# Performance work log

Measured on AMD Instinct MI355X. Metric: run time of the kernel, lower is better.

The kernel has to match this reference:

```python
import jax, jax.numpy as jnp
import numpy as np
from math import log, sqrt

B, S, D, H, L = 16, 512, 512, 8, 6
DPH = D // H
DFF = 2048
VOCAB = 1024
MAXDEG = 64
NPC, NS = 4096, 4096


def setup_inputs() -> dict:
    rng = np.random.default_rng(0)
    raw_x = rng.integers(0, VOCAB + 1, (B, S)).astype(np.int32)
    scatter_degree = rng.integers(0, MAXDEG + 1, (B, S)).astype(np.int32)

    def uniq_triples(n, seed):
        r = np.random.default_rng(seed)
        flat = r.choice(B * S * S, n, replace=False)  # unique (b,i,j)
        b, i, j = np.unravel_index(flat, (B, S, S))
        return np.stack([b, i, j], 1).astype(np.int32)

    parentchild_indices = uniq_triples(NPC, 1)
    silbing_indices = uniq_triples(NS, 2)
    parent_child_now = np.stack([np.arange(B), rng.integers(0, S, B)], 1).astype(np.int32)
    silbing_now = np.stack([np.arange(B), rng.integers(0, S, B)], 1).astype(np.int32)

    key = jax.random.key(0)
    ks = jax.random.split(key, 16)
    sc = 0.02
    inp = {
        "raw_x": jnp.asarray(raw_x),
        "scatter_degree": jnp.asarray(scatter_degree),
        "parentchild_indices": jnp.asarray(parentchild_indices),
        "parent_child_now": jnp.asarray(parent_child_now),
        "silbing_indices": jnp.asarray(silbing_indices),
        "silbing_now": jnp.asarray(silbing_now),
        "vocab_emb": jax.random.normal(ks[0], (VOCAB + 1, D), jnp.float32) * sc,
        "degree_emb": jax.random.normal(ks[1], (MAXDEG + 1, D), jnp.float32) * sc,
        "active_rel_emb": jax.random.normal(ks[2], (2, D), jnp.float32) * sc,
        "relation_encoder": jax.random.uniform(ks[3], (3,), jnp.float32),
        "Wq": jax.random.normal(ks[4], (L, D, D), jnp.float32) * sc,
        "bq": jnp.zeros((L, D), jnp.float32),
        "Wk": jax.random.normal(ks[5], (L, D, D), jnp.float32) * sc,
        "bk": jnp.zeros((L, D), jnp.float32),
        "Wv": jax.random.normal(ks[6], (L, D, D), jnp.float32) * sc,
        "bv": jnp.zeros((L, D), jnp.float32),
        "Wo": jax.random.normal(ks[7], (L, D, D), jnp.float32) * sc,
        "bo": jnp.zeros((L, D), jnp.float32),
        "W1": jax.random.normal(ks[8], (L, DFF, D), jnp.float32) * sc,
        "b1": jnp.zeros((L, DFF), jnp.float32),
        "W2": jax.random.normal(ks[9], (L, D, DFF), jnp.float32) * sc,
        "b2": jnp.zeros((L, D), jnp.float32),
        "ln_g": jnp.ones((L, D), jnp.float32),
        "ln_b": jnp.zeros((L, D), jnp.float32),
        "logits_w": jax.random.normal(ks[10], (VOCAB, D), jnp.float32) * sc,
    }
    return inp


def _layer_norm(x, g, b):
    m = jnp.mean(x, -1, keepdims=True)
    v = jnp.mean((x - m) ** 2, -1, keepdims=True)  # biased var, eps=1e-5 (torch default)
    return (x - m) * jax.lax.rsqrt(v + 1e-5) * g + b


def _forward(raw_x, scatter_degree, parentchild_indices, parent_child_now,
             silbing_indices, silbing_now, vocab_emb, degree_emb, active_rel_emb,
             relation_encoder, Wq, bq, Wk, bk, Wv, bv, Wo, bo, W1, b1, W2, b2,
             ln_g, ln_b, logits_w):
    x = vocab_emb[raw_x]  # [B,S,D]
    # sinusoidal positional encoding
    pos = jnp.arange(S, dtype=jnp.float32)[:, None]
    div = jnp.exp(jnp.arange(0, D, 2, dtype=jnp.float32) * (-log(10000.0) / D))
    pe = jnp.zeros((S, D), x.dtype).at[:, 0::2].set(jnp.sin(pos * div)).at[:, 1::2].set(jnp.cos(pos * div))
    x = x + pe
    # structural encodings
    x = x + degree_emb[scatter_degree]
    x = x.at[parent_child_now[:, 0], parent_child_now[:, 1]].add(active_rel_emb[0])
    x = x.at[silbing_now[:, 0], silbing_now[:, 1]].add(active_rel_emb[1])

    pb, pi, pj = parentchild_indices[:, 0], parentchild_indices[:, 1], parentchild_indices[:, 2]
    sb, si, sj = silbing_indices[:, 0], silbing_indices[:, 1], silbing_indices[:, 2]
    inv_norm = 1.0 / sqrt(DPH)

    for l in range(L):
        q = (x @ Wq[l].T + bq[l]).reshape(B, S, H, DPH).transpose(0, 2, 1, 3)
        k = (x @ Wk[l].T + bk[l]).reshape(B, S, H, DPH).transpose(0, 2, 1, 3)
        v = (x @ Wv[l].T + bv[l]).reshape(B, S, H, DPH).transpose(0, 2, 1, 3)
        scores = jnp.einsum('bhqd,bhkd->bhqk', q, k) * inv_norm  # [B,H,S,S]
        # scatter-added relational bias (broadcast over all heads)
        scores = scores.at[pb, :, pi, pj].add(relation_encoder[0])
        scores = scores.at[pb, :, pj, pi].add(relation_encoder[1])
        scores = scores.at[sb, :, si, sj].add(relation_encoder[2])
        scores = scores.at[sb, :, sj, si].add(relation_encoder[2])
        attn = jax.nn.softmax(scores, axis=-1)
        o = jnp.einsum('bhqk,bhkd->bhqd', attn, v).transpose(0, 2, 1, 3).reshape(B, S, D)
        o = o @ Wo[l].T + bo[l]
        x = _layer_norm(x + o, ln_g[l], ln_b[l])
        ff = jax.nn.relu(x @ W1[l].T + b1[l]) @ W2[l].T + b2[l]
        x = _layer_norm(x + ff, ln_g[l], ln_b[l])

    return x[:, -1] @ logits_w.T  # [B, VOCAB]


def reference(raw_x, scatter_degree, parentchild_indices, parent_child_now,
              silbing_indices, silbing_now, vocab_emb, degree_emb, active_rel_emb,
              relation_encoder, Wq, bq, Wk, bk, Wv, bv, Wo, bo, W1, b1, W2, b2,
              ln_g, ln_b, logits_w):
    return _forward(raw_x, scatter_degree, parentchild_indices, parent_child_now,
                    silbing_indices, silbing_now, vocab_emb, degree_emb, active_rel_emb,
                    relation_encoder, Wq, bq, Wk, bk, Wv, bv, Wo, bo, W1, b1, W2, b2,
                    ln_g, ln_b, logits_w)
```

## Files before the change

### kernel.cpp

```cpp
#include <hip/hip_runtime.h>
#include <hip/hip_bf16.h>
#include <math.h>

#define B_ 16
#define S_ 512
#define D_ 512
#define H_ 8
#define L_ 6
#define DPH_ 64
#define DFF_ 2048
#define VOCAB_ 1024
#define NPC_ 4096
#define NS_ 4096
#define BS_ (B_ * S_)
#define LOG2E 1.4426950408889634f

typedef __attribute__((ext_vector_type(8))) short bf16x8;
typedef __attribute__((ext_vector_type(4))) float f32x4;

__device__ __forceinline__ ushort f2bf(float f) {
    __hip_bfloat16 h = __float2bfloat16(f);
    return __builtin_bit_cast(ushort, h);
}
__device__ __forceinline__ float bf2f(ushort u) {
    unsigned int v = ((unsigned int)u) << 16;
    return __builtin_bit_cast(float, v);
}

__global__ __launch_bounds__(256) void embed_kernel(
    const int* __restrict__ raw_x, const int* __restrict__ sdeg,
    const float* __restrict__ vemb, const float* __restrict__ demb,
    ushort* __restrict__ xb)
{
    size_t idx = (size_t)blockIdx.x * 256 + threadIdx.x;
    int d = (int)(idx & (D_ - 1));
    size_t bs = idx >> 9;
    int s = (int)(bs & (S_ - 1));
    int tok = raw_x[bs];
    int dg  = sdeg[bs];
    float e = expf(-(float)(d & ~1) * (9.210340371976184f / (float)D_));
    float ang = (float)s * e;
    float pe = (d & 1) ? cosf(ang) : sinf(ang);
    xb[idx] = f2bf(vemb[(size_t)tok * D_ + d] + pe + demb[(size_t)dg * D_ + d]);
}

__global__ void relnow_kernel(const int* __restrict__ pcn, const int* __restrict__ sbn,
                              const float* __restrict__ arel, ushort* __restrict__ xb)
{
    int b = blockIdx.x;
    int t = threadIdx.x;
    int b1 = pcn[b * 2 + 0], p1 = pcn[b * 2 + 1];
    size_t i1 = ((size_t)(b1 * S_ + p1)) * D_ + t;
    xb[i1] = f2bf(bf2f(xb[i1]) + arel[t]);
    int b2 = sbn[b * 2 + 0], p2 = sbn[b * 2 + 1];
    size_t i2 = ((size_t)(b2 * S_ + p2)) * D_ + t;
    xb[i2] = f2bf(bf2f(xb[i2]) + arel[D_ + t]);
}

__global__ void bias_scatter_kernel(const int* __restrict__ pc, const int* __restrict__ sb,
                                    const float* __restrict__ renc, float* __restrict__ bias)
{
    int t = blockIdx.x * 256 + threadIdx.x;
    float r0 = renc[0], r1 = renc[1], r2 = renc[2];
    if (t < NPC_) {
        int b = pc[t * 3 + 0], i = pc[t * 3 + 1], j = pc[t * 3 + 2];
        atomicAdd(&bias[((size_t)b * S_ + i) * S_ + j], r0);
        atomicAdd(&bias[((size_t)b * S_ + j) * S_ + i], r1);
    } else if (t < NPC_ + NS_) {
        int u = t - NPC_;
        int b = sb[u * 3 + 0], i = sb[u * 3 + 1], j = sb[u * 3 + 2];
        atomicAdd(&bias[((size_t)b * S_ + i) * S_ + j], r2);
        atomicAdd(&bias[((size_t)b * S_ + j) * S_ + i], r2);
    }
}

__global__ __launch_bounds__(256) void bias_cast_kernel(const float* __restrict__ src,
                                                        ushort* __restrict__ dst)
{
    int i = blockIdx.x * 256 + threadIdx.x;
    float4 v = ((const float4*)src)[i];
    ushort4 o;
    o.x = f2bf(v.x * LOG2E); o.y = f2bf(v.y * LOG2E);
    o.z = f2bf(v.z * LOG2E); o.w = f2bf(v.w * LOG2E);
    ((ushort4*)dst)[i] = o;
}

__global__ __launch_bounds__(256) void cast4_kernel(const float* __restrict__ src,
                                                    ushort* __restrict__ dst, int n4)
{
    int i = blockIdx.x * 256 + threadIdx.x;
    if (i >= n4) return;
    float4 v = ((const float4*)src)[i];
    ushort4 o;
    o.x = f2bf(v.x); o.y = f2bf(v.y); o.z = f2bf(v.z); o.w = f2bf(v.w);
    ((ushort4*)dst)[i] = o;
}

__global__ __launch_bounds__(256) void pack_qkv_kernel(
    const float* __restrict__ Wq, const float* __restrict__ Wk, const float* __restrict__ Wv,
    ushort* __restrict__ dst)
{
    int idx = blockIdx.x * 256 + threadIdx.x;
    int c = idx & 511;
    int rl = idx >> 9;
    int r = rl % 1536, l = rl / 1536;
    float v;
    if (r < 512)       v = Wq[((size_t)l * 512 + r) * 512 + c];
    else if (r < 1024) v = Wk[((size_t)l * 512 + (r - 512)) * 512 + c];
    else               v = Wv[((size_t)l * 512 + (r - 1024)) * 512 + c];
    dst[idx] = f2bf(v);
}

__global__ void pack_bqkv_kernel(const float* __restrict__ bq, const float* __restrict__ bk,
                                 const float* __restrict__ bv, float* __restrict__ dst)
{
    int idx = blockIdx.x * 256 + threadIdx.x;
    if (idx >= L_ * 1536) return;
    int r = idx % 1536, l = idx / 1536;
    float v;
    if (r < 512)       v = bq[l * 512 + r];
    else if (r < 1024) v = bk[l * 512 + r - 512];
    else               v = bv[l * 512 + r - 1024];
    dst[idx] = v;
}

#define GL2LDS(g, l) __builtin_amdgcn_global_load_lds( \
    (const __attribute__((address_space(1))) void*)(g), \
    (__attribute__((address_space(3))) void*)(l), 16, 0, 0)

#define STAGE_AB(AsX, BsX, kk) do {                                            \
    _Pragma("unroll")                                                          \
    for (int i_ = 0; i_ < 2; i_++) {                                           \
        int r_ = i_ * 64 + wv * 16;                                            \
        GL2LDS(A + (size_t)(row0 + r_ + lr) * K + (kk) + lk, &AsX[r_ * 32]);   \
        GL2LDS(W + (size_t)(col0 + r_ + lr) * K + (kk) + lk, &BsX[r_ * 32]);   \
    } } while (0)

#define COMPUTE_AB(AsX, BsX) do {                                              \
    bf16x8 af[4], bf[4];                                                       \
    _Pragma("unroll")                                                          \
    for (int mi = 0; mi < 4; mi++)                                             \
        af[mi] = *(const bf16x8*)&AsX[(wm * 64 + mi * 16 + lc) * 32 + lq * 8]; \
    _Pragma("unroll")                                                          \
    for (int ni = 0; ni < 4; ni++)                                             \
        bf[ni] = *(const bf16x8*)&BsX[(wn * 64 + ni * 16 + lc) * 32 + lq * 8]; \
    _Pragma("unroll")                                                          \
    for (int mi = 0; mi < 4; mi++)                                             \
        _Pragma("unroll")                                                      \
        for (int ni = 0; ni < 4; ni++)                                         \
            acc[mi][ni] = __builtin_amdgcn_mfma_f32_16x16x32_bf16(af[mi], bf[ni], acc[mi][ni], 0, 0, 0); \
    } while (0)

__global__ __launch_bounds__(256) void gemm_bf16(
    const ushort* __restrict__ A, const ushort* __restrict__ W,
    const float* __restrict__ bias, ushort* __restrict__ Cb,
    int K, int M, int mode)
{
    __shared__ ushort As0[128 * 32];
    __shared__ ushort As1[128 * 32];
    __shared__ ushort Bs0[128 * 32];
    __shared__ ushort Bs1[128 * 32];

    const int t  = threadIdx.x;
    const int wv = t >> 6;
    const int ln = t & 63;
    const int wm = wv >> 1, wn = wv & 1;
    const int lq = ln >> 4, lc = ln & 15;
    const int row0 = blockIdx.x * 128;
    const int col0 = blockIdx.y * 128;
    const int lr = ln >> 2;
    const int lk = (ln & 3) * 8;

    f32x4 acc[4][4] = {};
    const int nk = K >> 5;

    STAGE_AB(As0, Bs0, 0);
    for (int ki = 0; ki < nk; ki += 2) {
        __syncthreads();
        if (ki + 1 < nk) STAGE_AB(As1, Bs1, (ki + 1) << 5);
        COMPUTE_AB(As0, Bs0);
        __syncthreads();
        if (ki + 2 < nk) STAGE_AB(As0, Bs0, (ki + 2) << 5);
        COMPUTE_AB(As1, Bs1);
    }

    #pragma unroll
    for (int mi = 0; mi < 4; mi++) {
        #pragma unroll
        for (int ni = 0; ni < 4; ni++) {
            int gcol = col0 + wn * 64 + ni * 16 + lc;
            float bb = bias[gcol];
            #pragma unroll
            for (int rr = 0; rr < 4; rr++) {
                int grow = row0 + wm * 64 + mi * 16 + lq * 4 + rr;
                float val = acc[mi][ni][rr] + bb;
                if (mode == 1) val = fmaxf(val, 0.f);
                Cb[(size_t)grow * M + gcol] = f2bf(val);
            }
        }
    }
}

#define STAGE_A64(AsX, BsX, kk) do {                                           \
    _Pragma("unroll")                                                          \
    for (int i_ = 0; i_ < 2; i_++) {                                           \
        int r_ = i_ * 64 + wv * 16;                                            \
        GL2LDS(A + (size_t)(row0 + r_ + lr) * K + (kk) + lk, &AsX[r_ * 32]);   \
    }                                                                          \
    {                                                                          \
        int rb_ = wv * 16;                                                     \
        GL2LDS(W + (size_t)(col0 + rb_ + lr) * K + (kk) + lk, &BsX[rb_ * 32]); \
    } } while (0)

#define COMPUTE_A64(AsX, BsX) do {                                             \
    bf16x8 af[4], bf[2];                                                       \
    _Pragma("unroll")                                                          \
    for (int mi = 0; mi < 4; mi++)                                             \
        af[mi] = *(const bf16x8*)&AsX[(wm * 64 + mi * 16 + lc) * 32 + lq * 8]; \
    _Pragma("unroll")                                                          \
    for (int ni = 0; ni < 2; ni++)                                             \
        bf[ni] = *(const bf16x8*)&BsX[(wn * 32 + ni * 16 + lc) * 32 + lq * 8]; \
    _Pragma("unroll")                                                          \
    for (int mi = 0; mi < 4; mi++)                                             \
        _Pragma("unroll")                                                      \
        for (int ni = 0; ni < 2; ni++)                                         \
            acc[mi][ni] = __builtin_amdgcn_mfma_f32_16x16x32_bf16(af[mi], bf[ni], acc[mi][ni], 0, 0, 0); \
    } while (0)

__global__ __launch_bounds__(256) void gemm64(
    const ushort* __restrict__ A, const ushort* __restrict__ W,
    ushort* __restrict__ Cb, int K, int M)
{
    __shared__ ushort As0[128 * 32];
    __shared__ ushort As1[128 * 32];
    __shared__ ushort Bs0[64 * 32];
    __shared__ ushort Bs1[64 * 32];

    const int t  = threadIdx.x;
    const int wv = t >> 6;
    const int ln = t & 63;
    const int wm = wv >> 1, wn = wv & 1;
    const int lq = ln >> 4, lc = ln & 15;
    const int row0 = blockIdx.x * 128;
    const int col0 = blockIdx.y * 64;
    const int lr = ln >> 2;
    const int lk = (ln & 3) * 8;

    f32x4 acc[4][2] = {};
    const int nk = K >> 5;

    STAGE_A64(As0, Bs0, 0);
    for (int ki = 0; ki < nk; ki += 2) {
        __syncthreads();
        if (ki + 1 < nk) STAGE_A64(As1, Bs1, (ki + 1) << 5);
        COMPUTE_A64(As0, Bs0);
        __syncthreads();
        if (ki + 2 < nk) STAGE_A64(As0, Bs0, (ki + 2) << 5);
        COMPUTE_A64(As1, Bs1);
    }

    #pragma unroll
    for (int mi = 0; mi < 4; mi++)
        #pragma unroll
        for (int ni = 0; ni < 2; ni++) {
            int gcol = col0 + wn * 32 + ni * 16 + lc;
            #pragma unroll
            for (int rr = 0; rr < 4; rr++) {
                int grow = row0 + wm * 64 + mi * 16 + lq * 4 + rr;
                Cb[(size_t)grow * M + gcol] = f2bf(acc[mi][ni][rr]);
            }
        }
}

#define PSTR 72

__device__ __forceinline__ int vswz(int d, int j) {
    int g = ((j >> 3) ^ (d & 7) ^ ((d >> 3) & 7)) & 7;
    return d * 64 + g * 8 + (j & 7);
}

#define ATTN_SUB(KsX, VtsX, jbase) do {                                        \
    f32x4 sf[4] = {};                                                          \
    _Pragma("unroll")                                                          \
    for (int ni = 0; ni < 4; ni++) {                                           \
        bf16x8 bk0 = *(const bf16x8*)&KsX[(ni * 16 + lc) * PSTR + lq * 8];     \
        bf16x8 bk1 = *(const bf16x8*)&KsX[(ni * 16 + lc) * PSTR + 32 + lq * 8];\
        sf[ni] = __builtin_amdgcn_mfma_f32_16x16x32_bf16(aq0, bk0, sf[ni], 0, 0, 0); \
        sf[ni] = __builtin_amdgcn_mfma_f32_16x16x32_bf16(aq1, bk1, sf[ni], 0, 0, 0); \
    }                                                                          \
    const ushort* bbase = biasb + (size_t)(b * S_ + i0 + wq * 16 + lq * 4) * S_ + (jbase); \
    _Pragma("unroll")                                                          \
    for (int ni = 0; ni < 4; ni++)                                             \
        _Pragma("unroll")                                                      \
        for (int rr = 0; rr < 4; rr++) {                                       \
            float bv = bf2f(bbase[(size_t)rr * S_ + ni * 16 + lc]);            \
            float p = __builtin_amdgcn_exp2f(fmaf(sf[ni][rr], QSC, bv));       \
            l_lane[rr] += p;                                                   \
            Ps[(wq * 16 + lq * 4 + rr) * PSTR + ni * 16 + lc] = f2bf(p);       \
        }                                                                      \
    bf16x8 ap0 = *(const bf16x8*)&Ps[(wq * 16 + lc) * PSTR + lq * 8];          \
    bf16x8 ap1 = *(const bf16x8*)&Ps[(wq * 16 + lc) * PSTR + 32 + lq * 8];     \
    _Pragma("unroll")                                                          \
    for (int ni = 0; ni < 4; ni++) {                                           \
        bf16x8 bv0 = *(const bf16x8*)&VtsX[vswz(ni * 16 + lc, lq * 8)];        \
        bf16x8 bv1 = *(const bf16x8*)&VtsX[vswz(ni * 16 + lc, 32 + lq * 8)];   \
        of[ni] = __builtin_amdgcn_mfma_f32_16x16x32_bf16(ap0, bv0, of[ni], 0, 0, 0); \
        of[ni] = __builtin_amdgcn_mfma_f32_16x16x32_bf16(ap1, bv1, of[ni], 0, 0, 0); \
    } } while (0)

__global__ __launch_bounds__(256) void attn_kernel(
    const ushort* __restrict__ qkv, const ushort* __restrict__ biasb,
    ushort* __restrict__ ao)
{
    const int qt = blockIdx.x, h = blockIdx.y, b = blockIdx.z;
    const int t  = threadIdx.x;
    const int wq = t >> 6;
    const int ln = t & 63;
    const int lq = ln >> 4;
    const int lc = ln & 15;
    const int r  = t >> 2;
    const int cg = t & 3;

    __shared__ ushort Qs[64 * PSTR];
    __shared__ ushort Ks0[64 * PSTR];
    __shared__ ushort Ks1[64 * PSTR];
    __shared__ ushort Ps[64 * PSTR];
    __shared__ ushort Vts0[64 * 64];
    __shared__ ushort Vts1[64 * 64];

    const int i0 = qt * 64;

    {
        const ushort* qsrc = qkv + (size_t)(b * S_ + i0 + r) * 1536 + h * 64 + cg * 16;
        *(uint4*)&Qs[r * PSTR + cg * 16]     = ((const uint4*)qsrc)[0];
        *(uint4*)&Qs[r * PSTR + cg * 16 + 8] = ((const uint4*)qsrc)[1];
    }
    bf16x8 aq0 = *(const bf16x8*)&Qs[(wq * 16 + lc) * PSTR + lq * 8];
    bf16x8 aq1 = *(const bf16x8*)&Qs[(wq * 16 + lc) * PSTR + 32 + lq * 8];

    f32x4 of[4] = {};
    float l_lane[4] = {};
    const float QSC = 0.125f * LOG2E;

    for (int j0 = 0; j0 < S_; j0 += 128) {
        __syncthreads();
        {
            const ushort* ksrc0 = qkv + (size_t)(b * S_ + j0 + r) * 1536 + 512 + h * 64 + cg * 16;
            const ushort* ksrc1 = ksrc0 + (size_t)64 * 1536;
            *(uint4*)&Ks0[r * PSTR + cg * 16]     = ((const uint4*)ksrc0)[0];
            *(uint4*)&Ks0[r * PSTR + cg * 16 + 8] = ((const uint4*)ksrc0)[1];
            *(uint4*)&Ks1[r * PSTR + cg * 16]     = ((const uint4*)ksrc1)[0];
            *(uint4*)&Ks1[r * PSTR + cg * 16 + 8] = ((const uint4*)ksrc1)[1];
            ushort vv[16];
            *(uint4*)&vv[0] = ((const uint4*)(ksrc0 + 512))[0];
            *(uint4*)&vv[8] = ((const uint4*)(ksrc0 + 512))[1];
            #pragma unroll
            for (int dd = 0; dd < 16; dd++)
                Vts0[vswz(cg * 16 + dd, r)] = vv[dd];
            *(uint4*)&vv[0] = ((const uint4*)(ksrc1 + 512))[0];
            *(uint4*)&vv[8] = ((const uint4*)(ksrc1 + 512))[1];
            #pragma unroll
            for (int dd = 0; dd < 16; dd++)
                Vts1[vswz(cg * 16 + dd, r)] = vv[dd];
        }
        __syncthreads();

        ATTN_SUB(Ks0, Vts0, j0);
        ATTN_SUB(Ks1, Vts1, j0 + 64);
    }

    float inv[4];
    #pragma unroll
    for (int rr = 0; rr < 4; rr++) {
        float s = l_lane[rr];
        s += __shfl_xor(s, 1);
        s += __shfl_xor(s, 2);
        s += __shfl_xor(s, 4);
        s += __shfl_xor(s, 8);
        inv[rr] = 1.f / s;
    }
    #pragma unroll
    for (int ni = 0; ni < 4; ni++)
        #pragma unroll
        for (int rr = 0; rr < 4; rr++) {
            int row = i0 + wq * 16 + lq * 4 + rr;
            ao[(size_t)(b * S_ + row) * D_ + h * 64 + ni * 16 + lc] = f2bf(of[ni][rr] * inv[rr]);
        }
}

__device__ __forceinline__ float block_sum(float v, float* red) {
    #pragma unroll
    for (int off = 32; off > 0; off >>= 1) v += __shfl_down(v, off);
    int t = threadIdx.x;
    if ((t & 63) == 0) red[t >> 6] = v;
    __syncthreads();
    float r = red[0] + red[1] + red[2] + red[3];
    __syncthreads();
    return r;
}

__global__ __launch_bounds__(256) void add_ln_kernel(
    ushort* __restrict__ xb, const ushort* __restrict__ pb,
    const float* __restrict__ bvec,
    const float* __restrict__ g, const float* __restrict__ bta)
{
    __shared__ float red[4];
    const int row = blockIdx.x;
    const int t = threadIdx.x;
    const size_t base = (size_t)row * D_;
    float v0 = bf2f(xb[base + t])       + bf2f(pb[base + t])       + bvec[t];
    float v1 = bf2f(xb[base + t + 256]) + bf2f(pb[base + t + 256]) + bvec[t + 256];
    float mean = block_sum(v0 + v1, red) * (1.f / (float)D_);
    float d0 = v0 - mean, d1 = v1 - mean;
    float var = block_sum(d0 * d0 + d1 * d1, red) * (1.f / (float)D_);
    float inv = rsqrtf(var + 1e-5f);
    float o0 = d0 * inv * g[t] + bta[t];
    float o1 = d1 * inv * g[t + 256] + bta[t + 256];
    xb[base + t]       = f2bf(o0);
    xb[base + t + 256] = f2bf(o1);
}

__global__ __launch_bounds__(256) void logits_kernel(
    const ushort* __restrict__ xb, const float* __restrict__ lw, float* __restrict__ out)
{
    __shared__ float xs[D_];
    const int b = blockIdx.x;
    const int vchunk = blockIdx.y;
    const int t = threadIdx.x;
    const ushort* xrow = xb + ((size_t)(b * S_ + (S_ - 1)) * D_);
    xs[t] = bf2f(xrow[t]);
    xs[t + 256] = bf2f(xrow[t + 256]);
    __syncthreads();
    for (int vv = vchunk * 128 + t; vv < vchunk * 128 + 128; vv += 256) {
        const float* wr = lw + (size_t)vv * D_;
        float acc = 0.f;
        #pragma unroll 8
        for (int d = 0; d < D_; d += 4) {
            float4 w4 = *(const float4*)&wr[d];
            acc += xs[d] * w4.x + xs[d + 1] * w4.y + xs[d + 2] * w4.z + xs[d + 3] * w4.w;
        }
        out[(size_t)b * VOCAB_ + vv] = acc;
    }
}

extern "C" void kernel_launch(void* const* d_in, const int* in_sizes, int n_in,
                              void* d_out, int out_size, void* d_ws, size_t ws_size,
                              hipStream_t stream)
{
    const int* raw_x = (const int*)d_in[0];
    const int* sdeg  = (const int*)d_in[1];
    const int* pci   = (const int*)d_in[2];
    const int* pcn   = (const int*)d_in[3];
    const int* sbi   = (const int*)d_in[4];
    const int* sbn   = (const int*)d_in[5];
    const float* vemb = (const float*)d_in[6];
    const float* demb = (const float*)d_in[7];
    const float* arel = (const float*)d_in[8];
    const float* renc = (const float*)d_in[9];
    const float* Wq = (const float*)d_in[10];
    const float* bq = (const float*)d_in[11];
    const float* Wk = (const float*)d_in[12];
    const float* bk = (const float*)d_in[13];
    const float* Wv = (const float*)d_in[14];
    const float* bv = (const float*)d_in[15];
    const float* Wo = (const float*)d_in[16];
    const float* bo = (const float*)d_in[17];
    const float* W1 = (const float*)d_in[18];
    const float* b1 = (const float*)d_in[19];
    const float* W2 = (const float*)d_in[20];
    const float* b2 = (const float*)d_in[21];
    const float* lng = (const float*)d_in[22];
    const float* lnb = (const float*)d_in[23];
    const float* lw  = (const float*)d_in[24];
    float* out = (float*)d_out;

    float* wsf = (float*)d_ws;
    const size_t X = (size_t)BS_ * D_;
    ushort* xb   = (ushort*)wsf;
    ushort* qkvb = (ushort*)(wsf + X / 2);
    ushort* ao   = (ushort*)(wsf + 2 * X);
    ushort* h1   = (ushort*)(wsf + (X * 5) / 2);
    ushort* projb= (ushort*)(wsf + (X * 9) / 2);
    float*  bias = wsf + 5 * X;
    ushort* biasb= (ushort*)(wsf + 6 * X);
    ushort* wb   = (ushort*)(wsf + (X * 13) / 2);
    ushort* wqkv_b = wb;
    ushort* wo_b   = wb + 4718592;
    ushort* w1_b   = wb + 6291456;
    ushort* w2_b   = wb + 12582912;
    float*  bqkv   = wsf + (X * 13) / 2 + 9437184;

    embed_kernel<<<(B_ * S_ * D_) / 256, 256, 0, stream>>>(raw_x, sdeg, vemb, demb, xb);
    relnow_kernel<<<B_, D_, 0, stream>>>(pcn, sbn, arel, xb);

    hipMemsetAsync(bias, 0, (size_t)B_ * S_ * S_ * sizeof(float), stream);
    bias_scatter_kernel<<<(NPC_ + NS_ + 255) / 256, 256, 0, stream>>>(pci, sbi, renc, bias);
    bias_cast_kernel<<<(B_ * S_ * S_ / 4) / 256, 256, 0, stream>>>(bias, biasb);

    pack_qkv_kernel<<<(L_ * 1536 * 512) / 256, 256, 0, stream>>>(Wq, Wk, Wv, wqkv_b);
    pack_bqkv_kernel<<<(L_ * 1536 + 255) / 256, 256, 0, stream>>>(bq, bk, bv, bqkv);
    cast4_kernel<<<(L_ * 512 * 512) / 4 / 256, 256, 0, stream>>>(Wo, wo_b, L_ * 512 * 512 / 4);
    cast4_kernel<<<(L_ * 2048 * 512) / 4 / 256, 256, 0, stream>>>(W1, w1_b, L_ * 2048 * 512 / 4);
    cast4_kernel<<<(L_ * 512 * 2048) / 4 / 256, 256, 0, stream>>>(W2, w2_b, L_ * 512 * 2048 / 4);

    dim3 blk(256);
    for (int l = 0; l < L_; l++) {
        gemm_bf16<<<dim3(BS_ / 128, 1536 / 128), blk, 0, stream>>>(
            xb, wqkv_b + (size_t)l * 1536 * 512, bqkv + l * 1536, qkvb, 512, 1536, 2);

        attn_kernel<<<dim3(S_ / 64, H_, B_), blk, 0, stream>>>(qkvb, biasb, ao);

        gemm64<<<dim3(BS_ / 128, 512 / 64), blk, 0, stream>>>(
            ao, wo_b + (size_t)l * 512 * 512, projb, 512, 512);
        add_ln_kernel<<<BS_, blk, 0, stream>>>(xb, projb, bo + l * 512,
                                               lng + l * D_, lnb + l * D_);

        gemm_bf16<<<dim3(BS_ / 128, 2048 / 128), blk, 0, stream>>>(
            xb, w1_b + (size_t)l * 2048 * 512, b1 + l * 2048, h1, 512, 2048, 1);
        gemm64<<<dim3(BS_ / 128, 512 / 64), blk, 0, stream>>>(
            h1, w2_b + (size_t)l * 512 * 2048, projb, 2048, 512);
        add_ln_kernel<<<BS_, blk, 0, stream>>>(xb, projb, b2 + l * 512,
                                               lng + l * D_, lnb + l * D_);
    }

    logits_kernel<<<dim3(B_, 8), blk, 0, stream>>>(xb, lw, out);
}
```

Baseline: 1.030 ms.

## Compute only the last token's query path in the final layer

The output depends only on the last sequence position, so in the final layer the full K/V projection still runs, but the query, attention, output projection, FFN and layer norms are computed for that single row per batch. Matrix-vector kernels replace the full GEMMs for those stages. This removes roughly five-sixths of the last layer's work in exchange for several small, latency-bound launches.

```diff
diff --git a/kernel.cpp b/kernel.cpp
--- a/kernel.cpp
+++ b/kernel.cpp
@@ -418,6 +418,103 @@
     float o1 = d1 * inv * g[t + 256] + bta[t + 256];
     xb[base + t]       = f2bf(o0);
     xb[base + t + 256] = f2bf(o1);
+}
+
+__global__ __launch_bounds__(256) void gemm_last(
+    const ushort* __restrict__ A, int aStride, int aOff,
+    const ushort* __restrict__ W, const float* __restrict__ bias,
+    ushort* __restrict__ C, int K, int M, int relu)
+{
+    __shared__ ushort as_[2048];
+    const int b  = blockIdx.y;
+    const int m0 = blockIdx.x * 64;
+    const int t  = threadIdx.x;
+    const ushort* arow = A + (size_t)b * aStride + aOff;
+    for (int k = t * 8; k < K; k += 2048)
+        *(uint4*)&as_[k] = *(const uint4*)&arow[k];
+    __syncthreads();
+    const int col = m0 + (t >> 2);
+    const int kl  = t & 3;
+    const int kq  = K >> 2;
+    const ushort* wrow = W + (size_t)col * K + kl * kq;
+    const ushort* ar   = &as_[kl * kq];
+    float acc = 0.f;
+    for (int k = 0; k < kq; k += 8) {
+        ushort uw[8], ua[8];
+        *(uint4*)uw = *(const uint4*)&wrow[k];
+        *(uint4*)ua = *(const uint4*)&ar[k];
+        #pragma unroll
+        for (int i = 0; i < 8; i++) acc += bf2f(ua[i]) * bf2f(uw[i]);
+    }
+    acc += __shfl_xor(acc, 1);
+    acc += __shfl_xor(acc, 2);
+    if (kl == 0) {
+        float val = acc + bias[col];
+        if (relu) val = fmaxf(val, 0.f);
+        C[(size_t)b * M + col] = f2bf(val);
+    }
+}
+
+__global__ __launch_bounds__(256) void attn_last_kernel(
+    const ushort* __restrict__ ql, const ushort* __restrict__ kv,
+    const ushort* __restrict__ biasb, ushort* __restrict__ ao16)
+{
+    const int h = blockIdx.x, b = blockIdx.y;
+    const int t = threadIdx.x;
+    __shared__ float qs[64];
+    __shared__ float sc[512];
+    __shared__ float red[4];
+    __shared__ float po[4][64];
+    if (t < 64) qs[t] = bf2f(ql[b * 512 + h * 64 + t]);
+    __syncthreads();
+    const float QSC = 0.125f * LOG2E;
+    const ushort* brow = biasb + ((size_t)(b * S_ + S_ - 1)) * S_;
+    float psum = 0.f;
+    for (int j = t; j < 512; j += 256) {
+        const ushort* krow = kv + ((size_t)(b * S_ + j)) * 1024 + h * 64;
+        float acc = 0.f;
+        #pragma unroll
+        for (int d8 = 0; d8 < 8; d8++) {
+            ushort uk[8];
+            *(uint4*)uk = ((const uint4*)krow)[d8];
+            #pragma unroll
+            for (int i = 0; i < 8; i++) acc += qs[d8 * 8 + i] * bf2f(uk[i]);
+        }
+        float p = __builtin_amdgcn_exp2f(fmaf(acc, QSC, bf2f(brow[j])));
+        sc[j] = p;
+        psum += p;
+    }
+    float inv = 1.f / block_sum(psum, red);
+    const int d = t & 63, c = t >> 6;
+    float acc = 0.f;
+    const ushort* vbase = kv + (size_t)(b * S_) * 1024 + 512 + h * 64 + d;
+    for (int j = c * 128; j < c * 128 + 128; j++)
+        acc += sc[j] * bf2f(vbase[(size_t)j * 1024]);
+    po[c][d] = acc;
+    __syncthreads();
+    if (t < 64) {
+        float r = (po[0][t] + po[1][t] + po[2][t] + po[3][t]) * inv;
+        ao16[b * 512 + h * 64 + t] = f2bf(r);
+    }
+}
+
+__global__ __launch_bounds__(256) void ln_last_kernel(
+    ushort* __restrict__ xb, const ushort* __restrict__ p16,
+    const float* __restrict__ g, const float* __restrict__ bta)
+{
+    __shared__ float red[4];
+    const int b = blockIdx.x;
+    const int t = threadIdx.x;
+    const size_t bx = ((size_t)(b * S_ + S_ - 1)) * D_;
+    const size_t bp = (size_t)b * D_;
+    float v0 = bf2f(xb[bx + t])       + bf2f(p16[bp + t]);
+    float v1 = bf2f(xb[bx + t + 256]) + bf2f(p16[bp + t + 256]);
+    float mean = block_sum(v0 + v1, red) * (1.f / (float)D_);
+    float d0 = v0 - mean, d1 = v1 - mean;
+    float var = block_sum(d0 * d0 + d1 * d1, red) * (1.f / (float)D_);
+    float inv = rsqrtf(var + 1e-5f);
+    xb[bx + t]       = f2bf(d0 * inv * g[t] + bta[t]);
+    xb[bx + t + 256] = f2bf(d1 * inv * g[t + 256] + bta[t + 256]);
 }
 
 __global__ __launch_bounds__(256) void logits_kernel(
@@ -489,6 +586,10 @@
     ushort* w1_b   = wb + 6291456;
     ushort* w2_b   = wb + 12582912;
     float*  bqkv   = wsf + (X * 13) / 2 + 9437184;
+    ushort* ql16 = (ushort*)(bqkv + 16384);
+    ushort* ao16 = ql16 + 16 * 512;
+    ushort* p16  = ao16 + 16 * 512;
+    ushort* h1l  = p16  + 16 * 512;
 
     embed_kernel<<<(B_ * S_ * D_) / 256, 256, 0, stream>>>(raw_x, sdeg, vemb, demb, xb);
     relnow_kernel<<<B_, D_, 0, stream>>>(pcn, sbn, arel, xb);
@@ -504,7 +605,7 @@
     cast4_kernel<<<(L_ * 512 * 2048) / 4 / 256, 256, 0, stream>>>(W2, w2_b, L_ * 512 * 2048 / 4);
 
     dim3 blk(256);
-    for (int l = 0; l < L_; l++) {
+    for (int l = 0; l < L_ - 1; l++) {
         gemm_bf16<<<dim3(BS_ / 128, 1536 / 128), blk, 0, stream>>>(
             xb, wqkv_b + (size_t)l * 1536 * 512, bqkv + l * 1536, qkvb, 512, 1536, 2);
 
@@ -523,5 +624,25 @@
                                                lng + l * D_, lnb + l * D_);
     }
 
+    {
+        const int l = L_ - 1;
+        gemm_bf16<<<dim3(BS_ / 128, 1024 / 128), blk, 0, stream>>>(
+            xb, wqkv_b + (size_t)l * 1536 * 512 + (size_t)512 * 512,
+            bqkv + l * 1536 + 512, qkvb, 512, 1024, 2);
+        gemm_last<<<dim3(512 / 64, B_), blk, 0, stream>>>(
+            xb, S_ * D_, (S_ - 1) * D_,
+            wqkv_b + (size_t)l * 1536 * 512, bqkv + l * 1536, ql16, 512, 512, 0);
+        attn_last_kernel<<<dim3(H_, B_), blk, 0, stream>>>(ql16, qkvb, biasb, ao16);
+        gemm_last<<<dim3(512 / 64, B_), blk, 0, stream>>>(
+            ao16, 512, 0, wo_b + (size_t)l * 512 * 512, bo + l * 512, p16, 512, 512, 0);
+        ln_last_kernel<<<B_, blk, 0, stream>>>(xb, p16, lng + l * D_, lnb + l * D_);
+        gemm_last<<<dim3(2048 / 64, B_), blk, 0, stream>>>(
+            xb, S_ * D_, (S_ - 1) * D_,
+            w1_b + (size_t)l * 2048 * 512, b1 + l * 2048, h1l, 512, 2048, 1);
+        gemm_last<<<dim3(512 / 64, B_), blk, 0, stream>>>(
+            h1l, 2048, 0, w2_b + (size_t)l * 512 * 2048, b2 + l * 512, p16, 2048, 512, 0);
+        ln_last_kernel<<<B_, blk, 0, stream>>>(xb, p16, lng + l * D_, lnb + l * D_);
+    }
+
     logits_kernel<<<dim3(B_, 8), blk, 0, stream>>>(xb, lw, out);
 }
```

Measured after the change: 950.1 us. -7.8%, faster.
